# Optimization experiments

Measured on AMD Instinct MI355X. Metric: run time of the kernel, lower is better.

Reference implementation:

```python
import jax, jax.numpy as jnp
import numpy as np

NUM_EXPERTS = 8
CAPACITY_FACTOR = 1.0
MIN_CAPACITY = 4


def setup_inputs() -> dict:
    key = jax.random.key(0)
    k0, k1, k2, k3 = jax.random.split(key, 4)
    B, S, M, F, E = 4, 2048, 2048, 8192, NUM_EXPERTS
    return {
        "hidden_states": jax.random.normal(k0, (B, S, M), jnp.float32),
        "wg": jax.random.normal(k1, (M, E), jnp.float32) * 0.02,
        "w1": jax.random.normal(k2, (E, M, F), jnp.float32) * 0.02,
        "b1": jnp.zeros((E, F), jnp.float32),
        "w2": jax.random.normal(k3, (E, F, M), jnp.float32) * 0.02,
        "b2": jnp.zeros((E, M), jnp.float32),
    }


def reference(hidden_states, wg, w1, b1, w2, b2):
    B, S, M = hidden_states.shape
    E = NUM_EXPERTS
    T = B * S  # total tokens
    x = hidden_states.reshape(T, M)

    # ---- top-1 gating (DeepSpeed top1gating, no noise / no RTS) ----
    logits = x @ wg                                  # [T, E]
    gates = jax.nn.softmax(logits, axis=-1)          # [T, E]
    capacity = max(int(np.ceil(T / E * CAPACITY_FACTOR)), MIN_CAPACITY)

    idx1 = jnp.argmax(gates, axis=1)                 # [T]
    mask1 = jax.nn.one_hot(idx1, E, dtype=gates.dtype)  # [T, E]

    # position of each token within its expert's queue
    locations1 = jnp.cumsum(mask1, axis=0) - 1.0     # [T, E]

    # load-balancing aux loss (computed before capacity drop)
    me = jnp.mean(gates, axis=0)
    ce = jnp.mean(mask1, axis=0)
    l_aux = jnp.sum(me * ce) * E

    # drop tokens beyond capacity
    mask1 = mask1 * (locations1 < capacity).astype(mask1.dtype)
    locations1_s = jnp.sum(locations1 * mask1, axis=1).astype(jnp.int32)  # [T]

    gates1 = gates * mask1                           # [T, E], zero for dropped tokens
    loc_sc = jax.nn.one_hot(locations1_s, capacity, dtype=gates.dtype)    # [T, C]

    combine_weights = jnp.einsum("se,sc->sec", gates1, loc_sc)            # [T, E, C]
    dispatch_mask = (combine_weights > 0).astype(x.dtype)                  # [T, E, C]

    # ---- dispatch -> grouped-GEMM experts -> combine ----
    dispatched = jnp.einsum("sec,sm->ecm", dispatch_mask, x)              # [E, C, M]
    h = jax.nn.gelu(jnp.einsum("ecm,emf->ecf", dispatched, w1) + b1[:, None, :])
    expert_out = jnp.einsum("ecf,efm->ecm", h, w2) + b2[:, None, :]       # [E, C, M]

    out = jnp.einsum("sec,ecm->sm", combine_weights, expert_out)          # [T, M]
    return out.reshape(B, S, M), l_aux
```

## Files before the change

### kernel.cpp

```cpp
#include <hip/hip_runtime.h>
#include <hip/hip_bf16.h>
#include <math.h>

#define T_TOK 8192
#define M_DIM 2048
#define F_DIM 8192
#define E_NUM 8
#define CAP   1024

typedef unsigned short u16;
typedef __attribute__((ext_vector_type(8))) short short8;
typedef __attribute__((ext_vector_type(4))) float f32x4;

__device__ __forceinline__ u16 f2bf(float f){
  unsigned int x = __builtin_bit_cast(unsigned int, f);
  unsigned int lsb = (x >> 16) & 1u;
  x += 0x7fffu + lsb;
  return (u16)(x >> 16);
}
__device__ __forceinline__ unsigned int pack2(float a, float b){
  return (unsigned int)f2bf(a) | ((unsigned int)f2bf(b) << 16);
}

typedef __attribute__((address_space(3))) unsigned int lds_uint;
typedef __attribute__((address_space(1))) const unsigned int g_uint;
__device__ __forceinline__ void gl_lds16(const u16* g, u16* l){
  __builtin_amdgcn_global_load_lds((g_uint*)g, (lds_uint*)l, 16, 0, 0);
}
typedef __attribute__((address_space(3))) u16 lds_u16;
__device__ __forceinline__ unsigned int lds_off(u16* p){
  return (unsigned int)(unsigned long long)(lds_u16*)p;
}

__device__ __forceinline__ float gelu_tanh(float v){
  float u = 0.7978845608028654f * (v + 0.044715f * v * v * v);
  return 0.5f * v * (1.0f + tanhf(u));
}

__device__ __forceinline__ size_t tiled_off(int e, int n, int k, int nt128, int nkt){
  return ((((size_t)e * nt128 + (n >> 7)) * nkt + (k >> 6)) * 2 + ((k >> 5) & 1)) * 4096
         + (size_t)((n & 127) * 32 + ((((k >> 3) & 3) ^ ((n >> 1) & 3)) << 3) + (k & 7));
}

__global__ __launch_bounds__(256) void gating_kernel(
    const float* __restrict__ x, const float* __restrict__ wg,
    int* __restrict__ expert_id, float* __restrict__ gate_val,
    float* __restrict__ mepart)
{
  int wave = threadIdx.x >> 6, lane = threadIdx.x & 63;
  int t = blockIdx.x * 4 + wave;
  float acc[8];
  #pragma unroll
  for (int e = 0; e < 8; ++e) acc[e] = 0.f;
  const float* xr = x + (size_t)t * M_DIM;
  for (int i = lane; i < M_DIM; i += 64) {
    float xv = xr[i];
    const float4* wr = (const float4*)(wg + (size_t)i * 8);
    float4 w0 = wr[0], w1v = wr[1];
    acc[0] += xv * w0.x;  acc[1] += xv * w0.y;  acc[2] += xv * w0.z;  acc[3] += xv * w0.w;
    acc[4] += xv * w1v.x; acc[5] += xv * w1v.y; acc[6] += xv * w1v.z; acc[7] += xv * w1v.w;
  }
  #pragma unroll
  for (int off = 32; off; off >>= 1)
    #pragma unroll
    for (int e = 0; e < 8; ++e) acc[e] += __shfl_xor(acc[e], off);

  float mx = acc[0]; int bi = 0;
  #pragma unroll
  for (int e = 1; e < 8; ++e) if (acc[e] > mx) { mx = acc[e]; bi = e; }
  float p[8]; float s = 0.f;
  #pragma unroll
  for (int e = 0; e < 8; ++e) { p[e] = expf(acc[e] - mx); s += p[e]; }
  float inv = 1.f / s;

  __shared__ float pl[4][8];
  if (lane == 0) {
    expert_id[t] = bi;
    gate_val[t] = p[bi] * inv;
    #pragma unroll
    for (int e = 0; e < 8; ++e) pl[wave][e] = p[e] * inv;
  }
  __syncthreads();
  if (threadIdx.x < 8) {
    float m = pl[0][threadIdx.x] + pl[1][threadIdx.x] + pl[2][threadIdx.x] + pl[3][threadIdx.x];
    mepart[blockIdx.x * 8 + threadIdx.x] = m;
  }
}

__global__ __launch_bounds__(1024) void scan_kernel(
    const int* __restrict__ expert_id, const float* __restrict__ gate_val,
    const float* __restrict__ mepart, int nmep,
    int* __restrict__ slot_token, float* __restrict__ slot_gate,
    float* __restrict__ laux_out)
{
  __shared__ int wcnt[16][8];
  __shared__ int base[8];
  __shared__ float red[128][8];
  int tid = threadIdx.x, wave = tid >> 6, lane = tid & 63;
  if (tid < 8) base[tid] = 0;

  int e0 = tid & 7, g = tid >> 3;
  float mesum = 0.f;
  for (int r = g; r < nmep; r += 128) mesum += mepart[r * 8 + e0];
  red[g][e0] = mesum;
  __syncthreads();

  for (int tile = 0; tile < T_TOK / 1024; ++tile) {
    int t = tile * 1024 + tid;
    int e = expert_id[t];
    int lp = 0;
    #pragma unroll
    for (int ee = 0; ee < 8; ++ee) {
      unsigned long long m = __ballot(e == ee);
      if (lane == 0) wcnt[wave][ee] = __popcll(m);
      if (ee == e)   lp = __popcll(m & ((1ull << lane) - 1ull));
    }
    __syncthreads();
    int wp = 0;
    for (int w2 = 0; w2 < wave; ++w2) wp += wcnt[w2][e];
    int pos = base[e] + wp + lp;
    if (pos < CAP) {
      slot_token[e * CAP + pos] = t;
      slot_gate[e * CAP + pos] = gate_val[t];
    }
    __syncthreads();
    if (tid < 8) {
      int s = 0;
      for (int w2 = 0; w2 < 16; ++w2) s += wcnt[w2][tid];
      base[tid] += s;
    }
    __syncthreads();
  }

  if (tid < 8) {
    float me = 0.f;
    for (int r = 0; r < 128; ++r) me += red[r][tid];
    me /= (float)T_TOK;
    float ce = (float)base[tid] / (float)T_TOK;
    red[0][tid] = me * ce;
  }
  __syncthreads();
  if (tid == 0) {
    float s = 0.f;
    for (int e = 0; e < 8; ++e) s += red[0][e];
    *laux_out = s * (float)E_NUM;
  }
}

__global__ __launch_bounds__(256) void transpose_cvt_kernel(
    const float* __restrict__ in, u16* __restrict__ out, int R, int Cc)
{
  __shared__ float tile[64][65];
  int e = blockIdx.z;
  const float* ine = in + (size_t)e * R * Cc;
  int r0 = blockIdx.y * 64, c0 = blockIdx.x * 64;
  int tr = threadIdx.x >> 4, tc = threadIdx.x & 15;
  #pragma unroll
  for (int it = 0; it < 4; ++it) {
    float4 v = *(const float4*)&ine[(size_t)(r0 + it * 16 + tr) * Cc + c0 + tc * 4];
    tile[it * 16 + tr][tc * 4 + 0] = v.x;
    tile[it * 16 + tr][tc * 4 + 1] = v.y;
    tile[it * 16 + tr][tc * 4 + 2] = v.z;
    tile[it * 16 + tr][tc * 4 + 3] = v.w;
  }
  __syncthreads();
  int nt128 = Cc >> 7, nkt = R >> 6;
  int oc = threadIdx.x >> 2, q = threadIdx.x & 3;
  int n = c0 + oc, k0 = r0 + q * 16;
  u16 vals[16];
  #pragma unroll
  for (int i = 0; i < 16; ++i) vals[i] = f2bf(tile[q * 16 + i][oc]);
  unsigned int w[8];
  #pragma unroll
  for (int i = 0; i < 8; ++i) w[i] = (unsigned int)vals[2 * i] | ((unsigned int)vals[2 * i + 1] << 16);
  uint4 pa; pa.x = w[0]; pa.y = w[1]; pa.z = w[2]; pa.w = w[3];
  uint4 pb; pb.x = w[4]; pb.y = w[5]; pb.z = w[6]; pb.w = w[7];
  *(uint4*)&out[tiled_off(e, n, k0,     nt128, nkt)] = pa;
  *(uint4*)&out[tiled_off(e, n, k0 + 8, nt128, nkt)] = pb;
}

__global__ __launch_bounds__(256) void dispatch_kernel(
    const float* __restrict__ x, const int* __restrict__ slot_token,
    u16* __restrict__ Xe)
{
  int slot = blockIdx.x;
  int e = slot >> 10, c = slot & (CAP - 1);
  int t = slot_token[slot];
  int m = threadIdx.x * 8;
  uint4 pk;
  if (t < 0) {
    pk.x = pk.y = pk.z = pk.w = 0u;
  } else {
    const float* xr = x + (size_t)t * M_DIM + m;
    float4 a = *(const float4*)xr;
    float4 b = *(const float4*)(xr + 4);
    pk.x = pack2(a.x, a.y); pk.y = pack2(a.z, a.w);
    pk.z = pack2(b.x, b.y); pk.w = pack2(b.z, b.w);
  }
  *(uint4*)&Xe[tiled_off(e, c, m, CAP >> 7, M_DIM >> 6)] = pk;
}

template<int MH>
__device__ __forceinline__ void do_phase(
    unsigned aAddr, unsigned bAddr,
    short8 (&bfr)[4], f32x4 (&acc)[4][4],
    const u16* __restrict__ tb, u16* sreg, int skt,
    int tid, int wave)
{
  short8 af[2];
  unsigned aA = aAddr + MH * 2048;
  if (MH == 0) {
    asm volatile("ds_read_b128 %0, %1 offset:0"    : "=v"(bfr[0]) : "v"(bAddr));
    asm volatile("ds_read_b128 %0, %1 offset:1024" : "=v"(bfr[1]) : "v"(bAddr));
    asm volatile("ds_read_b128 %0, %1 offset:2048" : "=v"(bfr[2]) : "v"(bAddr));
    asm volatile("ds_read_b128 %0, %1 offset:3072" : "=v"(bfr[3]) : "v"(bAddr));
  }
  asm volatile("ds_read_b128 %0, %1 offset:0"    : "=v"(af[0]) : "v"(aA));
  asm volatile("ds_read_b128 %0, %1 offset:1024" : "=v"(af[1]) : "v"(aA));
  const u16* src = tb + ((size_t)skt << 12);
  #pragma unroll
  for (int j = 0; j < 2; ++j)
    gl_lds16(src + (size_t)(j * 256 + tid) * 8, sreg + (j * 256 + (wave << 6)) * 8);
  __builtin_amdgcn_s_barrier();
  asm volatile("s_waitcnt lgkmcnt(0)");
  __builtin_amdgcn_sched_barrier(0);
  __builtin_amdgcn_s_setprio(1);
  #pragma unroll
  for (int m2 = 0; m2 < 2; ++m2)
    #pragma unroll
    for (int n2 = 0; n2 < 4; ++n2)
      acc[MH * 2 + m2][n2] = __builtin_amdgcn_mfma_f32_16x16x32_bf16(
          af[m2], bfr[n2], acc[MH * 2 + m2][n2], 0, 0, 0);
  __builtin_amdgcn_s_setprio(0);
  if (MH == 1) {
    asm volatile("s_waitcnt vmcnt(2)");
    __builtin_amdgcn_sched_barrier(0);
  }
  __builtin_amdgcn_s_barrier();
}

template<int EPI>
__global__ __launch_bounds__(256, 4) void gemm8_kernel(
    const u16* __restrict__ A,
    const u16* __restrict__ B,
    const float* __restrict__ bias,
    u16* __restrict__ Hout,
    float* __restrict__ Out,
    const int* __restrict__ slot_token, const float* __restrict__ slot_gate,
    int K, int NR)
{
  __shared__ __align__(16) u16 SA[2][4096];
  __shared__ __align__(16) u16 SB[2][4096];

  int e = blockIdx.z;
  int n0 = blockIdx.x * 128, m0 = blockIdx.y * 128;
  int nreg = K >> 5;
  const u16* Atb = A + ((size_t)(e * (CAP >> 7) + (m0 >> 7)) * nreg) * 4096;
  const u16* Btb = B + ((size_t)(e * (NR >> 7) + (n0 >> 7)) * nreg) * 4096;

  int tid = threadIdx.x, wave = tid >> 6, lane = tid & 63;
  int wr = wave >> 1, wc = wave & 1;
  int l15 = lane & 15, g2 = lane >> 4;

  int rs = (l15 >> 1) & 3;
  int cg = (g2 ^ rs) * 8;
  int arow_base = (wr * 64 + l15) * 32 + cg;
  int brow_base = (wc * 64 + l15) * 32 + cg;

  unsigned aAddr[2], bAddr[2];
  #pragma unroll
  for (int b = 0; b < 2; ++b) {
    aAddr[b] = lds_off(&SA[b][0]) + (unsigned)(arow_base * 2);
    bAddr[b] = lds_off(&SB[b][0]) + (unsigned)(brow_base * 2);
  }

  f32x4 acc[4][4];
  #pragma unroll
  for (int m = 0; m < 4; ++m)
    #pragma unroll
    for (int n = 0; n < 4; ++n)
      acc[m][n] = (f32x4){0.f, 0.f, 0.f, 0.f};
  short8 bfr[4];

  auto stageR = [&](const u16* tb, u16* region, int kt) {
    const u16* src = tb + ((size_t)kt << 12);
    #pragma unroll
    for (int j = 0; j < 2; ++j)
      gl_lds16(src + (size_t)(j * 256 + tid) * 8, region + (j * 256 + (wave << 6)) * 8);
  };

  int nk = K >> 5;
  stageR(Atb, &SA[0][0], 0);
  stageR(Btb, &SB[0][0], 0);
  stageR(Btb, &SB[1][0], 1);
  asm volatile("s_waitcnt vmcnt(2)");
  __builtin_amdgcn_sched_barrier(0);
  __builtin_amdgcn_s_barrier();

  #pragma unroll 1
  for (int t = 0; t < nk; ++t) {
    int p = t & 1;
    int tA = t + 1 < nk ? t + 1 : nk - 1;
    int tB = t + 2 < nk ? t + 2 : nk - 1;
    do_phase<0>(aAddr[p], bAddr[p], bfr, acc, Atb, &SA[p ^ 1][0], tA, tid, wave);
    do_phase<1>(aAddr[p], bAddr[p], bfr, acc, Btb, &SB[p][0], tB, tid, wave);
  }

  int wrb = wr * 64, wcb = wc * 64;
  const float* be = bias + (size_t)e * NR + n0;
  if (EPI == 0) {
    #pragma unroll
    for (int wm = 0; wm < 4; ++wm) {
      #pragma unroll
      for (int j = 0; j < 4; ++j) {
        int r = wrb + wm * 16 + g2 * 4 + j;
        #pragma unroll
        for (int n = 0; n < 4; ++n) {
          int c = wcb + n * 16 + l15;
          float v = acc[wm][n][j] + be[c];
          Hout[tiled_off(e, m0 + r, n0 + c, CAP >> 7, F_DIM >> 6)] = f2bf(gelu_tanh(v));
        }
      }
    }
  } else {
    #pragma unroll
    for (int wm = 0; wm < 4; ++wm) {
      #pragma unroll
      for (int j = 0; j < 4; ++j) {
        int r = wrb + wm * 16 + g2 * 4 + j;
        int slot = e * CAP + m0 + r;
        int tk = slot_token[slot];
        if (tk >= 0) {
          float gv = slot_gate[slot];
          size_t rowoff = (size_t)tk * M_DIM + n0;
          #pragma unroll
          for (int n = 0; n < 4; ++n) {
            int c = wcb + n * 16 + l15;
            Out[rowoff + c] = gv * (acc[wm][n][j] + be[c]);
          }
        }
      }
    }
  }
}

extern "C" void kernel_launch(void* const* d_in, const int* in_sizes, int n_in,
                              void* d_out, int out_size, void* d_ws, size_t ws_size,
                              hipStream_t stream) {
  const float* x  = (const float*)d_in[0];
  const float* wg = (const float*)d_in[1];
  const float* w1 = (const float*)d_in[2];
  const float* b1 = (const float*)d_in[3];
  const float* w2 = (const float*)d_in[4];
  const float* b2 = (const float*)d_in[5];
  float* out = (float*)d_out;

  char* ws = (char*)d_ws;
  size_t o = 0;
  auto alloc = [&](size_t bytes) -> void* {
    void* p = ws + o;
    o += (bytes + 255) & ~(size_t)255;
    return p;
  };
  u16*   w1T        = (u16*)  alloc((size_t)E_NUM * F_DIM * M_DIM * 2);
  u16*   w2T        = (u16*)  alloc((size_t)E_NUM * M_DIM * F_DIM * 2);
  u16*   h          = (u16*)  alloc((size_t)E_NUM * CAP * F_DIM * 2);
  u16*   Xe         = (u16*)  alloc((size_t)E_NUM * CAP * M_DIM * 2);
  int*   expert_id  = (int*)  alloc(T_TOK * 4);
  float* gate_val   = (float*)alloc(T_TOK * 4);
  int*   slot_token = (int*)  alloc(E_NUM * CAP * 4);
  float* slot_gate  = (float*)alloc(E_NUM * CAP * 4);
  float* mepart     = (float*)alloc(2048 * 8 * 4);

  hipMemsetAsync(d_out, 0, (size_t)out_size * 4, stream);
  hipMemsetAsync(slot_token, 0xFF, E_NUM * CAP * 4, stream);

  gating_kernel<<<T_TOK / 4, 256, 0, stream>>>(x, wg, expert_id, gate_val, mepart);
  scan_kernel<<<1, 1024, 0, stream>>>(expert_id, gate_val, mepart, 2048,
                                      slot_token, slot_gate, out + (out_size - 1));
  transpose_cvt_kernel<<<dim3(128, 32, 8), 256, 0, stream>>>(w1, w1T, 2048, 8192);
  transpose_cvt_kernel<<<dim3(32, 128, 8), 256, 0, stream>>>(w2, w2T, 8192, 2048);
  dispatch_kernel<<<E_NUM * CAP, 256, 0, stream>>>(x, slot_token, Xe);

  gemm8_kernel<0><<<dim3(F_DIM / 128, CAP / 128, E_NUM), 256, 0, stream>>>(
      Xe, w1T, b1, h, nullptr, nullptr, nullptr, M_DIM, F_DIM);
  gemm8_kernel<1><<<dim3(M_DIM / 128, CAP / 128, E_NUM), 256, 0, stream>>>(
      h, w2T, b2, nullptr, out, slot_token, slot_gate, F_DIM, M_DIM);
}
```

Before: 981.2 us.

## Enlarge GEMM tiles to 256x128 with 512 threads and triple-buffered A

Expert GEMMs now use a 256-row M tile with 8 waves per block, so each B tile loaded into LDS is shared by twice as many rows. A is triple-buffered and B double-buffered, and the pipeline loop is rewritten inline instead of using the two-phase helper. The activation and hidden tensors move to a 256-row tiled layout to match. The aim is less B-operand global traffic per FLOP, in exchange for more LDS per block, fewer blocks per grid, and possibly lower occupancy.

Result: faster. 943.9 us (-3.8%).

```diff
diff --git a/kernel.cpp b/kernel.cpp
--- a/kernel.cpp
+++ b/kernel.cpp
@@ -37,7 +37,11 @@
   return 0.5f * v * (1.0f + tanhf(u));
 }
 
-__device__ __forceinline__ size_t tiled_off(int e, int n, int k, int nt128, int nkt){
+__device__ __forceinline__ size_t tiled256(int e, int n, int k, int nt256, int nkt){
+  return ((((size_t)e * nt256 + (n >> 8)) * nkt + (k >> 6)) * 2 + ((k >> 5) & 1)) * 8192
+         + (size_t)((n & 255) * 32 + ((((k >> 3) & 3) ^ ((n >> 1) & 3)) << 3) + (k & 7));
+}
+__device__ __forceinline__ size_t tiled128(int e, int n, int k, int nt128, int nkt){
   return ((((size_t)e * nt128 + (n >> 7)) * nkt + (k >> 6)) * 2 + ((k >> 5) & 1)) * 4096
          + (size_t)((n & 127) * 32 + ((((k >> 3) & 3) ^ ((n >> 1) & 3)) << 3) + (k & 7));
 }
@@ -175,8 +179,8 @@
   for (int i = 0; i < 8; ++i) w[i] = (unsigned int)vals[2 * i] | ((unsigned int)vals[2 * i + 1] << 16);
   uint4 pa; pa.x = w[0]; pa.y = w[1]; pa.z = w[2]; pa.w = w[3];
   uint4 pb; pb.x = w[4]; pb.y = w[5]; pb.z = w[6]; pb.w = w[7];
-  *(uint4*)&out[tiled_off(e, n, k0,     nt128, nkt)] = pa;
-  *(uint4*)&out[tiled_off(e, n, k0 + 8, nt128, nkt)] = pb;
+  *(uint4*)&out[tiled128(e, n, k0,     nt128, nkt)] = pa;
+  *(uint4*)&out[tiled128(e, n, k0 + 8, nt128, nkt)] = pb;
 }
 
 __global__ __launch_bounds__(256) void dispatch_kernel(
@@ -197,50 +201,11 @@
     pk.x = pack2(a.x, a.y); pk.y = pack2(a.z, a.w);
     pk.z = pack2(b.x, b.y); pk.w = pack2(b.z, b.w);
   }
-  *(uint4*)&Xe[tiled_off(e, c, m, CAP >> 7, M_DIM >> 6)] = pk;
-}
-
-template<int MH>
-__device__ __forceinline__ void do_phase(
-    unsigned aAddr, unsigned bAddr,
-    short8 (&bfr)[4], f32x4 (&acc)[4][4],
-    const u16* __restrict__ tb, u16* sreg, int skt,
-    int tid, int wave)
-{
-  short8 af[2];
-  unsigned aA = aAddr + MH * 2048;
-  if (MH == 0) {
-    asm volatile("ds_read_b128 %0, %1 offset:0"    : "=v"(bfr[0]) : "v"(bAddr));
-    asm volatile("ds_read_b128 %0, %1 offset:1024" : "=v"(bfr[1]) : "v"(bAddr));
-    asm volatile("ds_read_b128 %0, %1 offset:2048" : "=v"(bfr[2]) : "v"(bAddr));
-    asm volatile("ds_read_b128 %0, %1 offset:3072" : "=v"(bfr[3]) : "v"(bAddr));
-  }
-  asm volatile("ds_read_b128 %0, %1 offset:0"    : "=v"(af[0]) : "v"(aA));
-  asm volatile("ds_read_b128 %0, %1 offset:1024" : "=v"(af[1]) : "v"(aA));
-  const u16* src = tb + ((size_t)skt << 12);
-  #pragma unroll
-  for (int j = 0; j < 2; ++j)
-    gl_lds16(src + (size_t)(j * 256 + tid) * 8, sreg + (j * 256 + (wave << 6)) * 8);
-  __builtin_amdgcn_s_barrier();
-  asm volatile("s_waitcnt lgkmcnt(0)");
-  __builtin_amdgcn_sched_barrier(0);
-  __builtin_amdgcn_s_setprio(1);
-  #pragma unroll
-  for (int m2 = 0; m2 < 2; ++m2)
-    #pragma unroll
-    for (int n2 = 0; n2 < 4; ++n2)
-      acc[MH * 2 + m2][n2] = __builtin_amdgcn_mfma_f32_16x16x32_bf16(
-          af[m2], bfr[n2], acc[MH * 2 + m2][n2], 0, 0, 0);
-  __builtin_amdgcn_s_setprio(0);
-  if (MH == 1) {
-    asm volatile("s_waitcnt vmcnt(2)");
-    __builtin_amdgcn_sched_barrier(0);
-  }
-  __builtin_amdgcn_s_barrier();
+  *(uint4*)&Xe[tiled256(e, c, m, CAP >> 8, M_DIM >> 6)] = pk;
 }
 
 template<int EPI>
-__global__ __launch_bounds__(256, 4) void gemm8_kernel(
+__global__ __launch_bounds__(512, 4) void gemmk(
     const u16* __restrict__ A,
     const u16* __restrict__ B,
     const float* __restrict__ bias,
@@ -249,14 +214,14 @@
     const int* __restrict__ slot_token, const float* __restrict__ slot_gate,
     int K, int NR)
 {
-  __shared__ __align__(16) u16 SA[2][4096];
+  __shared__ __align__(16) u16 SA[3][8192];
   __shared__ __align__(16) u16 SB[2][4096];
 
   int e = blockIdx.z;
-  int n0 = blockIdx.x * 128, m0 = blockIdx.y * 128;
-  int nreg = K >> 5;
-  const u16* Atb = A + ((size_t)(e * (CAP >> 7) + (m0 >> 7)) * nreg) * 4096;
-  const u16* Btb = B + ((size_t)(e * (NR >> 7) + (n0 >> 7)) * nreg) * 4096;
+  int n0 = blockIdx.x * 128, m0 = blockIdx.y * 256;
+  int nkt = K >> 6;
+  const u16* Atb = A + (((size_t)(e * (CAP >> 8) + (m0 >> 8)) * nkt) * 2) * 8192;
+  const u16* Btb = B + (((size_t)(e * (NR >> 7) + (n0 >> 7)) * nkt) * 2) * 4096;
 
   int tid = threadIdx.x, wave = tid >> 6, lane = tid & 63;
   int wr = wave >> 1, wc = wave & 1;
@@ -267,12 +232,11 @@
   int arow_base = (wr * 64 + l15) * 32 + cg;
   int brow_base = (wc * 64 + l15) * 32 + cg;
 
-  unsigned aAddr[2], bAddr[2];
-  #pragma unroll
-  for (int b = 0; b < 2; ++b) {
-    aAddr[b] = lds_off(&SA[b][0]) + (unsigned)(arow_base * 2);
-    bAddr[b] = lds_off(&SB[b][0]) + (unsigned)(brow_base * 2);
-  }
+  unsigned aAddr[3], bAddr[2];
+  #pragma unroll
+  for (int b = 0; b < 3; ++b) aAddr[b] = lds_off(&SA[b][0]) + (unsigned)(arow_base * 2);
+  #pragma unroll
+  for (int b = 0; b < 2; ++b) bAddr[b] = lds_off(&SB[b][0]) + (unsigned)(brow_base * 2);
 
   f32x4 acc[4][4];
   #pragma unroll
@@ -282,28 +246,71 @@
       acc[m][n] = (f32x4){0.f, 0.f, 0.f, 0.f};
   short8 bfr[4];
 
-  auto stageR = [&](const u16* tb, u16* region, int kt) {
-    const u16* src = tb + ((size_t)kt << 12);
+  auto stageA = [&](u16* region, int reg) {
+    const u16* src = Atb + ((size_t)reg << 13);
     #pragma unroll
     for (int j = 0; j < 2; ++j)
-      gl_lds16(src + (size_t)(j * 256 + tid) * 8, region + (j * 256 + (wave << 6)) * 8);
+      gl_lds16(src + (size_t)(j * 512 + tid) * 8, region + (j * 512 + (wave << 6)) * 8);
   };
+  auto stageB = [&](u16* region, int reg) {
+    const u16* src = Btb + ((size_t)reg << 12);
+    gl_lds16(src + (size_t)tid * 8, region + (size_t)(wave << 6) * 8);
+  };
 
   int nk = K >> 5;
-  stageR(Atb, &SA[0][0], 0);
-  stageR(Btb, &SB[0][0], 0);
-  stageR(Btb, &SB[1][0], 1);
+  stageB(&SB[0][0], 0);
+  stageA(&SA[0][0], 0);
+  stageA(&SA[1][0], 1);
   asm volatile("s_waitcnt vmcnt(2)");
   __builtin_amdgcn_sched_barrier(0);
   __builtin_amdgcn_s_barrier();
 
+  int ia = 0, ib = 0;
   #pragma unroll 1
   for (int t = 0; t < nk; ++t) {
-    int p = t & 1;
-    int tA = t + 1 < nk ? t + 1 : nk - 1;
-    int tB = t + 2 < nk ? t + 2 : nk - 1;
-    do_phase<0>(aAddr[p], bAddr[p], bfr, acc, Atb, &SA[p ^ 1][0], tA, tid, wave);
-    do_phase<1>(aAddr[p], bAddr[p], bfr, acc, Btb, &SB[p][0], tB, tid, wave);
+    int ia2 = ia + 2 >= 3 ? ia - 1 : ia + 2;
+    int ib1 = ib ^ 1;
+    int rb = t + 1 < nk ? t + 1 : nk - 1;
+    int ra = t + 2 < nk ? t + 2 : nk - 1;
+    short8 af[2];
+    asm volatile("ds_read_b128 %0, %1 offset:0"    : "=v"(bfr[0]) : "v"(bAddr[ib]));
+    asm volatile("ds_read_b128 %0, %1 offset:1024" : "=v"(bfr[1]) : "v"(bAddr[ib]));
+    asm volatile("ds_read_b128 %0, %1 offset:2048" : "=v"(bfr[2]) : "v"(bAddr[ib]));
+    asm volatile("ds_read_b128 %0, %1 offset:3072" : "=v"(bfr[3]) : "v"(bAddr[ib]));
+    asm volatile("ds_read_b128 %0, %1 offset:0"    : "=v"(af[0]) : "v"(aAddr[ia]));
+    asm volatile("ds_read_b128 %0, %1 offset:1024" : "=v"(af[1]) : "v"(aAddr[ia]));
+    stageB(&SB[ib1][0], rb);
+    stageA(&SA[ia2][0], ra);
+    __builtin_amdgcn_s_barrier();
+    asm volatile("s_waitcnt lgkmcnt(0)");
+    __builtin_amdgcn_sched_barrier(0);
+    __builtin_amdgcn_s_setprio(1);
+    #pragma unroll
+    for (int m2 = 0; m2 < 2; ++m2)
+      #pragma unroll
+      for (int n2 = 0; n2 < 4; ++n2)
+        acc[m2][n2] = __builtin_amdgcn_mfma_f32_16x16x32_bf16(
+            af[m2], bfr[n2], acc[m2][n2], 0, 0, 0);
+    __builtin_amdgcn_s_setprio(0);
+    __builtin_amdgcn_s_barrier();
+    asm volatile("ds_read_b128 %0, %1 offset:2048" : "=v"(af[0]) : "v"(aAddr[ia]));
+    asm volatile("ds_read_b128 %0, %1 offset:3072" : "=v"(af[1]) : "v"(aAddr[ia]));
+    __builtin_amdgcn_s_barrier();
+    asm volatile("s_waitcnt lgkmcnt(0)");
+    __builtin_amdgcn_sched_barrier(0);
+    __builtin_amdgcn_s_setprio(1);
+    #pragma unroll
+    for (int m2 = 0; m2 < 2; ++m2)
+      #pragma unroll
+      for (int n2 = 0; n2 < 4; ++n2)
+        acc[2 + m2][n2] = __builtin_amdgcn_mfma_f32_16x16x32_bf16(
+            af[m2], bfr[n2], acc[2 + m2][n2], 0, 0, 0);
+    __builtin_amdgcn_s_setprio(0);
+    asm volatile("s_waitcnt vmcnt(2)");
+    __builtin_amdgcn_sched_barrier(0);
+    __builtin_amdgcn_s_barrier();
+    ia = ia + 1 >= 3 ? 0 : ia + 1;
+    ib = ib1;
   }
 
   int wrb = wr * 64, wcb = wc * 64;
@@ -318,7 +325,7 @@
         for (int n = 0; n < 4; ++n) {
           int c = wcb + n * 16 + l15;
           float v = acc[wm][n][j] + be[c];
-          Hout[tiled_off(e, m0 + r, n0 + c, CAP >> 7, F_DIM >> 6)] = f2bf(gelu_tanh(v));
+          Hout[tiled256(e, m0 + r, n0 + c, CAP >> 8, F_DIM >> 6)] = f2bf(gelu_tanh(v));
         }
       }
     }
@@ -382,8 +389,8 @@
   transpose_cvt_kernel<<<dim3(32, 128, 8), 256, 0, stream>>>(w2, w2T, 8192, 2048);
   dispatch_kernel<<<E_NUM * CAP, 256, 0, stream>>>(x, slot_token, Xe);
 
-  gemm8_kernel<0><<<dim3(F_DIM / 128, CAP / 128, E_NUM), 256, 0, stream>>>(
+  gemmk<0><<<dim3(F_DIM / 128, CAP / 256, E_NUM), 512, 0, stream>>>(
       Xe, w1T, b1, h, nullptr, nullptr, nullptr, M_DIM, F_DIM);
-  gemm8_kernel<1><<<dim3(M_DIM / 128, CAP / 128, E_NUM), 256, 0, stream>>>(
+  gemmk<1><<<dim3(M_DIM / 128, CAP / 256, E_NUM), 512, 0, stream>>>(
       h, w2T, b2, nullptr, out, slot_token, slot_gate, F_DIM, M_DIM);
 }
```
